# Optimization experiments

Measured on AMD Instinct MI355X. Metric: run time of the kernel, lower is better.

The kernel has to match this reference:

```python
import jax, jax.numpy as jnp
import numpy as np

# DeltaNet single-token decode step. Hard-coded dims from the torch source:
# hidden H=2048 (chosen), qk=2048 (16h x 128 -> repeat to 32h), v=4096 (32h x 128),
# conv channels 8192, kernel 4, state [1,32,128,128].
H = 2048
EPS = 1e-6

def _l2norm(x):
    return x * jax.lax.rsqrt(jnp.sum(x * x, axis=-1, keepdims=True) + EPS)

def setup_inputs() -> dict:
    key = jax.random.key(0)
    ks = jax.random.split(key, 12)
    w = lambda k, s, sc=0.02: jax.random.normal(k, s, dtype=jnp.float32) * sc
    return {
        "x": jax.random.normal(ks[0], (1, 1, H), dtype=jnp.float32),
        "state": jax.random.normal(ks[1], (1, 32, 128, 128), dtype=jnp.float32) * 0.02,
        "conv_state": jax.random.normal(ks[2], (1, 8192, 3), dtype=jnp.float32) * 0.1,
        "W_qkv": w(ks[3], (8192, H)),
        "W_z": w(ks[4], (4096, H)),
        "W_b": w(ks[5], (32, H)),
        "W_a": w(ks[6], (32, H)),
        "conv_w": w(ks[7], (8192, 1, 4), 0.3),
        "A_log": jax.random.uniform(ks[8], (32,), minval=-2.0, maxval=0.0, dtype=jnp.float32),
        "dt_bias": w(ks[9], (32,), 0.5),
        "norm_w": jnp.ones((128,), jnp.float32),
        "W_out": w(ks[10], (H, 4096)),
    }

def reference(x, state, conv_state, W_qkv, W_z, W_b, W_a, conv_w, A_log, dt_bias, norm_w, W_out):
    # projections (bias-free Linear, torch convention y = x @ W.T)
    mixed = jnp.einsum('blh,ch->blc', x, W_qkv)           # [1,1,8192]
    z = jnp.einsum('blh,ch->blc', x, W_z).reshape(1, 1, 32, 128)
    beta = jax.nn.sigmoid(jnp.einsum('blh,ch->blc', x, W_b))  # [1,1,32]
    a = jnp.einsum('blh,ch->blc', x, W_a)                 # [1,1,32]

    # depthwise causal conv (groups=8192, kernel 4, output length 1)
    combined = jnp.concatenate([conv_state, mixed.transpose(0, 2, 1)], axis=-1)  # [1,8192,4]
    new_conv = combined[:, :, -3:]
    conv_out = jnp.sum(combined * conv_w[None, :, 0, :], axis=-1)  # [1,8192]
    mixed = jax.nn.silu(conv_out)[:, None, :]             # [1,1,8192]

    q, k, v = mixed[..., :2048], mixed[..., 2048:4096], mixed[..., 4096:]
    q = jnp.repeat(q.reshape(1, 1, 16, 128), 2, axis=2)   # [1,1,32,128]
    k = jnp.repeat(k.reshape(1, 1, 16, 128), 2, axis=2)
    v = v.reshape(1, 1, 32, 128)

    g = -jnp.exp(A_log) * jax.nn.softplus(a + dt_bias)    # [1,1,32]

    q = _l2norm(q)[:, 0] / jnp.sqrt(jnp.float32(128.0))   # [1,32,128]
    k = _l2norm(k)[:, 0]
    v = v[:, 0]
    g_t = jnp.exp(g[:, 0])[..., None, None]               # [1,32,1,1]
    beta_t = beta[:, 0][..., None]                        # [1,32,1]

    # gated delta-rule state update
    s = state * g_t                                       # [1,32,128,128]
    kv_mem = jnp.einsum('bhkv,bhk->bhv', s, k)            # [1,32,128]
    delta = (v - kv_mem) * beta_t
    new_state = s + k[..., None] * delta[..., None, :]    # [1,32,128,128]
    out = jnp.einsum('bhkv,bhk->bhv', new_state, q)       # [1,32,128]

    # gated RMSNorm (Mamba2-style: rmsnorm(x * silu(z)) * w)
    out_flat = out.reshape(-1, 128)
    z_flat = z.reshape(-1, 128)
    gated = out_flat * jax.nn.silu(z_flat)
    out_flat = gated * jax.lax.rsqrt(jnp.mean(gated * gated, axis=-1, keepdims=True) + EPS) * norm_w

    out = jnp.einsum('blc,hc->blh', out_flat.reshape(1, 1, 4096), W_out)  # [1,1,H]
    return (out, new_state, new_conv)
```

## Files before the change

### kernel.cpp

```cpp
#include <hip/hip_runtime.h>
#include <math.h>

__device__ __forceinline__ float silu(float x){ return x / (1.f + expf(-x)); }

__global__ __launch_bounds__(256) void k_gemv_in(
    const float* __restrict__ x,
    const float* __restrict__ Wqkv,
    const float* __restrict__ Wz,
    const float* __restrict__ Wb,
    const float* __restrict__ Wa,
    float* __restrict__ mixed, float* __restrict__ zb,
    float* __restrict__ b_raw, float* __restrict__ a_raw)
{
  const int tid  = threadIdx.x;
  const int lane = tid & 63;
  const int wave = tid >> 6;

  float4 xr[8];
  #pragma unroll
  for (int j = 0; j < 8; j++)
    xr[j] = *(const float4*)(x + j*256 + lane*4);

  const int row0 = blockIdx.x * 8 + wave * 2;
  const float* W; float* dst;
  if (row0 < 8192)       { W = Wqkv + (size_t)row0 * 2048;          dst = mixed + row0; }
  else if (row0 < 12288) { W = Wz   + (size_t)(row0-8192) * 2048;   dst = zb + (row0-8192); }
  else if (row0 < 12320) { W = Wb   + (size_t)(row0-12288) * 2048;  dst = b_raw + (row0-12288); }
  else                   { W = Wa   + (size_t)(row0-12320) * 2048;  dst = a_raw + (row0-12320); }

  float acc0 = 0.f, acc1 = 0.f;
  #pragma unroll
  for (int j = 0; j < 8; j++){
    float4 w0 = *(const float4*)(W + j*256 + lane*4);
    float4 w1 = *(const float4*)(W + 2048 + j*256 + lane*4);
    acc0 += w0.x*xr[j].x + w0.y*xr[j].y + w0.z*xr[j].z + w0.w*xr[j].w;
    acc1 += w1.x*xr[j].x + w1.y*xr[j].y + w1.z*xr[j].z + w1.w*xr[j].w;
  }
  #pragma unroll
  for (int off = 32; off >= 1; off >>= 1){
    acc0 += __shfl_xor(acc0, off, 64);
    acc1 += __shfl_xor(acc1, off, 64);
  }
  if (lane == 0){ dst[0] = acc0; dst[1] = acc1; }
}

__global__ __launch_bounds__(256) void k_head(
    const float* __restrict__ mixed,
    const float* __restrict__ conv_state,
    const float* __restrict__ conv_w,
    const float* __restrict__ zbuf,
    const float* __restrict__ b_raw,
    const float* __restrict__ a_raw,
    const float* __restrict__ A_log,
    const float* __restrict__ dt_bias,
    const float* __restrict__ norm_w,
    const float* __restrict__ state,
    const float* __restrict__ Wout,
    float* __restrict__ new_state,
    float* __restrict__ new_conv,
    float* __restrict__ out_flat,
    float* __restrict__ scratch)
{
  const int b   = blockIdx.x;
  const int tid = threadIdx.x;

  if (b >= 32){
    const float4* W4 = (const float4*)Wout + (size_t)b * 8192;
    float4 a = make_float4(0.f, 0.f, 0.f, 0.f);
    #pragma unroll
    for (int j = 0; j < 32; j++){
      float4 w = W4[j*256 + tid];
      a.x += w.x; a.y += w.y; a.z += w.z; a.w += w.w;
    }
    if (tid == 0) scratch[b] = a.x + a.y + a.z + a.w;
    return;
  }

  const int h  = b;
  const int hb = h >> 1;
  const int t  = tid & 127;
  const int lane = tid & 63, wid = tid >> 6;

  __shared__ float qn[128], kn[128];
  __shared__ __align__(16) float vs[128];
  __shared__ float4 kvp[8][32];
  __shared__ float red[4];

  float qv = 0.f, kv = 0.f;
  if (tid < 128){
    int c = hb*128 + t;
    float c0 = conv_state[c*3+0], c1 = conv_state[c*3+1], c2 = conv_state[c*3+2];
    float m  = mixed[c];
    qv = silu(c0*conv_w[c*4+0] + c1*conv_w[c*4+1] + c2*conv_w[c*4+2] + m*conv_w[c*4+3]);
    new_conv[c*3+0] = c1; new_conv[c*3+1] = c2; new_conv[c*3+2] = m;
    c = 2048 + hb*128 + t;
    c0 = conv_state[c*3+0]; c1 = conv_state[c*3+1]; c2 = conv_state[c*3+2];
    m  = mixed[c];
    kv = silu(c0*conv_w[c*4+0] + c1*conv_w[c*4+1] + c2*conv_w[c*4+2] + m*conv_w[c*4+3]);
    new_conv[c*3+0] = c1; new_conv[c*3+1] = c2; new_conv[c*3+2] = m;

    float sq = qv*qv, sk = kv*kv;
    #pragma unroll
    for (int off = 32; off >= 1; off >>= 1){
      sq += __shfl_xor(sq, off, 64);
      sk += __shfl_xor(sk, off, 64);
    }
    if (lane == 0){ red[wid] = sq; red[2+wid] = sk; }
  } else {
    int c = 4096 + h*128 + t;
    float c0 = conv_state[c*3+0], c1 = conv_state[c*3+1], c2 = conv_state[c*3+2];
    float m  = mixed[c];
    vs[t] = silu(c0*conv_w[c*4+0] + c1*conv_w[c*4+1] + c2*conv_w[c*4+2] + m*conv_w[c*4+3]);
    new_conv[c*3+0] = c1; new_conv[c*3+1] = c2; new_conv[c*3+2] = m;
  }
  __syncthreads();
  const float qscale = rsqrtf(red[0]+red[1] + 1e-6f) * 0.088388347648318440550f;
  const float kscale = rsqrtf(red[2]+red[3] + 1e-6f);
  if (tid < 128){ qn[t] = qv * qscale; kn[t] = kv * kscale; }
  __syncthreads();

  float g_t, beta;
  {
    const float av = a_raw[h] + dt_bias[h];
    const float sp = (av > 20.f) ? av : log1pf(expf(av));
    g_t  = expf(-expf(A_log[h]) * sp);
    beta = 1.f / (1.f + expf(-b_raw[h]));
  }

  const int cg = tid & 31, part = tid >> 5;
  const int k0 = part * 16;
  const float* st  = state     + (size_t)h * 16384;
  float*       nst = new_state + (size_t)h * 16384;

  float4 s4[16];
  float4 kvm = make_float4(0.f, 0.f, 0.f, 0.f);
  #pragma unroll
  for (int i = 0; i < 16; i++){
    float4 sv = *(const float4*)(st + (k0+i)*128 + cg*4);
    sv.x *= g_t; sv.y *= g_t; sv.z *= g_t; sv.w *= g_t;
    s4[i] = sv;
    const float kk = kn[k0+i];
    kvm.x += sv.x*kk; kvm.y += sv.y*kk; kvm.z += sv.z*kk; kvm.w += sv.w*kk;
  }
  kvp[part][cg] = kvm;
  __syncthreads();
  float4 kt = make_float4(0.f, 0.f, 0.f, 0.f);
  #pragma unroll
  for (int p = 0; p < 8; p++){
    float4 kp = kvp[p][cg];
    kt.x += kp.x; kt.y += kp.y; kt.z += kp.z; kt.w += kp.w;
  }
  const float4 v4 = *(const float4*)(vs + cg*4);
  float4 delta;
  delta.x = (v4.x - kt.x) * beta;
  delta.y = (v4.y - kt.y) * beta;
  delta.z = (v4.z - kt.z) * beta;
  delta.w = (v4.w - kt.w) * beta;

  float4 oacc = make_float4(0.f, 0.f, 0.f, 0.f);
  #pragma unroll
  for (int i = 0; i < 16; i++){
    const float kk = kn[k0+i];
    float4 ns;
    ns.x = s4[i].x + kk*delta.x;
    ns.y = s4[i].y + kk*delta.y;
    ns.z = s4[i].z + kk*delta.z;
    ns.w = s4[i].w + kk*delta.w;
    *(float4*)(nst + (k0+i)*128 + cg*4) = ns;
    const float qq = qn[k0+i];
    oacc.x += ns.x*qq; oacc.y += ns.y*qq; oacc.z += ns.z*qq; oacc.w += ns.w*qq;
  }
  __syncthreads();
  kvp[part][cg] = oacc;
  __syncthreads();
  if (part == 0){
    float4 o = make_float4(0.f, 0.f, 0.f, 0.f);
    #pragma unroll
    for (int p = 0; p < 8; p++){
      float4 op = kvp[p][cg];
      o.x += op.x; o.y += op.y; o.z += op.z; o.w += op.w;
    }
    const float4 z4 = *(const float4*)(zbuf + h*128 + cg*4);
    float4 g4;
    g4.x = o.x * silu(z4.x);
    g4.y = o.y * silu(z4.y);
    g4.z = o.z * silu(z4.z);
    g4.w = o.w * silu(z4.w);
    float s2 = g4.x*g4.x + g4.y*g4.y + g4.z*g4.z + g4.w*g4.w;
    #pragma unroll
    for (int off = 16; off >= 1; off >>= 1) s2 += __shfl_xor(s2, off, 64);
    const float r = rsqrtf(s2 * (1.f/128.f) + 1e-6f);
    const float4 nw = *(const float4*)(norm_w + cg*4);
    float4 ov;
    ov.x = g4.x * r * nw.x;
    ov.y = g4.y * r * nw.y;
    ov.z = g4.z * r * nw.z;
    ov.w = g4.w * r * nw.w;
    *(float4*)(out_flat + h*128 + cg*4) = ov;
  }
}

__global__ __launch_bounds__(256) void k_gemv_out(
    const float* __restrict__ out_flat,
    const float* __restrict__ Wout,
    float* __restrict__ out)
{
  __shared__ float xs[4096];
  const int tid = threadIdx.x;
  #pragma unroll
  for (int i = 0; i < 4; i++)
    *(float4*)(xs + tid*4 + i*1024) = *(const float4*)(out_flat + tid*4 + i*1024);
  __syncthreads();

  const int lane = tid & 63, wave = tid >> 6;
  const int row0 = blockIdx.x * 8 + wave * 2;
  const float* W0 = Wout + (size_t)row0 * 4096;
  float acc0 = 0.f, acc1 = 0.f;
  #pragma unroll
  for (int j = 0; j < 16; j++){
    float4 w0 = *(const float4*)(W0 + j*256 + lane*4);
    float4 w1 = *(const float4*)(W0 + 4096 + j*256 + lane*4);
    const float x0 = xs[j*256+lane*4+0], x1 = xs[j*256+lane*4+1];
    const float x2 = xs[j*256+lane*4+2], x3 = xs[j*256+lane*4+3];
    acc0 += w0.x*x0 + w0.y*x1 + w0.z*x2 + w0.w*x3;
    acc1 += w1.x*x0 + w1.y*x1 + w1.z*x2 + w1.w*x3;
  }
  #pragma unroll
  for (int off = 32; off >= 1; off >>= 1){
    acc0 += __shfl_xor(acc0, off, 64);
    acc1 += __shfl_xor(acc1, off, 64);
  }
  if (lane == 0){ out[row0] = acc0; out[row0+1] = acc1; }
}

extern "C" void kernel_launch(void* const* d_in, const int* in_sizes, int n_in,
                              void* d_out, int out_size, void* d_ws, size_t ws_size,
                              hipStream_t stream) {
  const float* x          = (const float*)d_in[0];
  const float* state      = (const float*)d_in[1];
  const float* conv_state = (const float*)d_in[2];
  const float* W_qkv      = (const float*)d_in[3];
  const float* W_z        = (const float*)d_in[4];
  const float* W_b        = (const float*)d_in[5];
  const float* W_a        = (const float*)d_in[6];
  const float* conv_w     = (const float*)d_in[7];
  const float* A_log      = (const float*)d_in[8];
  const float* dt_bias    = (const float*)d_in[9];
  const float* norm_w     = (const float*)d_in[10];
  const float* W_out      = (const float*)d_in[11];

  float* out       = (float*)d_out;
  float* new_state = (float*)d_out + 2048;
  float* new_conv  = (float*)d_out + 2048 + 524288;

  float* ws      = (float*)d_ws;
  float* mixed   = ws;
  float* zb      = ws + 8192;
  float* b_raw   = ws + 12288;
  float* a_raw   = ws + 12320;
  float* oflat   = ws + 12352;
  float* scratch = ws + 16448;

  hipLaunchKernelGGL(k_gemv_in, dim3(1544), dim3(256), 0, stream,
                     x, W_qkv, W_z, W_b, W_a, mixed, zb, b_raw, a_raw);
  hipLaunchKernelGGL(k_head, dim3(256), dim3(256), 0, stream,
                     mixed, conv_state, conv_w, zb, b_raw, a_raw, A_log, dt_bias,
                     norm_w, state, W_out, new_state, new_conv, oflat, scratch);
  hipLaunchKernelGGL(k_gemv_out, dim3(256), dim3(256), 0, stream,
                     oflat, W_out, out);
}
```

Baseline: 177.8 us.

## Fuse three decode kernels into one cooperative persistent kernel with grid syncs

Merges the input GEMV, the per-head delta-rule update and the output GEMV into a single cooperative kernel of 256 blocks, with grid-wide syncs between stages. The input GEMV becomes a grid-stride loop over rows, and the W_out prefetch-warming pass now runs in every block before the final stage. The goal is to remove the inter-kernel launch gaps and keep W_out warm in cache. The trade-off is that the first GEMV now runs on far fewer blocks (256 instead of 1544), which can limit memory parallelism, and the grid syncs add their own overhead.

```diff
diff --git a/kernel.cpp b/kernel.cpp
--- a/kernel.cpp
+++ b/kernel.cpp
@@ -1,236 +1,236 @@
 #include <hip/hip_runtime.h>
+#include <hip/hip_cooperative_groups.h>
 #include <math.h>
 
+namespace cg = cooperative_groups;
+
 __device__ __forceinline__ float silu(float x){ return x / (1.f + expf(-x)); }
 
-__global__ __launch_bounds__(256) void k_gemv_in(
+__global__ __launch_bounds__(256) void k_fused(
     const float* __restrict__ x,
-    const float* __restrict__ Wqkv,
-    const float* __restrict__ Wz,
-    const float* __restrict__ Wb,
-    const float* __restrict__ Wa,
-    float* __restrict__ mixed, float* __restrict__ zb,
-    float* __restrict__ b_raw, float* __restrict__ a_raw)
-{
-  const int tid  = threadIdx.x;
-  const int lane = tid & 63;
-  const int wave = tid >> 6;
-
-  float4 xr[8];
-  #pragma unroll
-  for (int j = 0; j < 8; j++)
-    xr[j] = *(const float4*)(x + j*256 + lane*4);
-
-  const int row0 = blockIdx.x * 8 + wave * 2;
-  const float* W; float* dst;
-  if (row0 < 8192)       { W = Wqkv + (size_t)row0 * 2048;          dst = mixed + row0; }
-  else if (row0 < 12288) { W = Wz   + (size_t)(row0-8192) * 2048;   dst = zb + (row0-8192); }
-  else if (row0 < 12320) { W = Wb   + (size_t)(row0-12288) * 2048;  dst = b_raw + (row0-12288); }
-  else                   { W = Wa   + (size_t)(row0-12320) * 2048;  dst = a_raw + (row0-12320); }
-
-  float acc0 = 0.f, acc1 = 0.f;
-  #pragma unroll
-  for (int j = 0; j < 8; j++){
-    float4 w0 = *(const float4*)(W + j*256 + lane*4);
-    float4 w1 = *(const float4*)(W + 2048 + j*256 + lane*4);
-    acc0 += w0.x*xr[j].x + w0.y*xr[j].y + w0.z*xr[j].z + w0.w*xr[j].w;
-    acc1 += w1.x*xr[j].x + w1.y*xr[j].y + w1.z*xr[j].z + w1.w*xr[j].w;
-  }
-  #pragma unroll
-  for (int off = 32; off >= 1; off >>= 1){
-    acc0 += __shfl_xor(acc0, off, 64);
-    acc1 += __shfl_xor(acc1, off, 64);
-  }
-  if (lane == 0){ dst[0] = acc0; dst[1] = acc1; }
-}
-
-__global__ __launch_bounds__(256) void k_head(
-    const float* __restrict__ mixed,
     const float* __restrict__ conv_state,
+    const float* __restrict__ W_qkv,
+    const float* __restrict__ W_z,
+    const float* __restrict__ W_b,
+    const float* __restrict__ W_a,
     const float* __restrict__ conv_w,
-    const float* __restrict__ zbuf,
-    const float* __restrict__ b_raw,
-    const float* __restrict__ a_raw,
     const float* __restrict__ A_log,
     const float* __restrict__ dt_bias,
     const float* __restrict__ norm_w,
     const float* __restrict__ state,
     const float* __restrict__ Wout,
+    float* __restrict__ out,
     float* __restrict__ new_state,
     float* __restrict__ new_conv,
-    float* __restrict__ out_flat,
+    float* __restrict__ mixed,
+    float* __restrict__ zb,
+    float* __restrict__ b_raw,
+    float* __restrict__ a_raw,
+    float* __restrict__ oflat,
     float* __restrict__ scratch)
 {
-  const int b   = blockIdx.x;
-  const int tid = threadIdx.x;
-
-  if (b >= 32){
-    const float4* W4 = (const float4*)Wout + (size_t)b * 8192;
-    float4 a = make_float4(0.f, 0.f, 0.f, 0.f);
-    #pragma unroll
-    for (int j = 0; j < 32; j++){
-      float4 w = W4[j*256 + tid];
-      a.x += w.x; a.y += w.y; a.z += w.z; a.w += w.w;
-    }
-    if (tid == 0) scratch[b] = a.x + a.y + a.z + a.w;
-    return;
-  }
-
-  const int h  = b;
-  const int hb = h >> 1;
-  const int t  = tid & 127;
-  const int lane = tid & 63, wid = tid >> 6;
+  cg::grid_group grid = cg::this_grid();
+  const int b    = blockIdx.x;
+  const int tid  = threadIdx.x;
+  const int lane = tid & 63;
+  const int wave = tid >> 6;
 
   __shared__ float qn[128], kn[128];
   __shared__ __align__(16) float vs[128];
   __shared__ float4 kvp[8][32];
   __shared__ float red[4];
-
-  float qv = 0.f, kv = 0.f;
-  if (tid < 128){
-    int c = hb*128 + t;
-    float c0 = conv_state[c*3+0], c1 = conv_state[c*3+1], c2 = conv_state[c*3+2];
-    float m  = mixed[c];
-    qv = silu(c0*conv_w[c*4+0] + c1*conv_w[c*4+1] + c2*conv_w[c*4+2] + m*conv_w[c*4+3]);
-    new_conv[c*3+0] = c1; new_conv[c*3+1] = c2; new_conv[c*3+2] = m;
-    c = 2048 + hb*128 + t;
-    c0 = conv_state[c*3+0]; c1 = conv_state[c*3+1]; c2 = conv_state[c*3+2];
-    m  = mixed[c];
-    kv = silu(c0*conv_w[c*4+0] + c1*conv_w[c*4+1] + c2*conv_w[c*4+2] + m*conv_w[c*4+3]);
-    new_conv[c*3+0] = c1; new_conv[c*3+1] = c2; new_conv[c*3+2] = m;
-
-    float sq = qv*qv, sk = kv*kv;
+  __shared__ __align__(16) float xs[4096];
+
+  {
+    float4 xr[8];
+    #pragma unroll
+    for (int j = 0; j < 8; j++)
+      xr[j] = *(const float4*)(x + j*256 + lane*4);
+
+    for (int row0 = (b*4 + wave)*2; row0 < 12352; row0 += 2048){
+      const float* W; float* dst;
+      if (row0 < 8192)       { W = W_qkv + (size_t)row0 * 2048;          dst = mixed + row0; }
+      else if (row0 < 12288) { W = W_z   + (size_t)(row0-8192) * 2048;   dst = zb + (row0-8192); }
+      else if (row0 < 12320) { W = W_b   + (size_t)(row0-12288) * 2048;  dst = b_raw + (row0-12288); }
+      else                   { W = W_a   + (size_t)(row0-12320) * 2048;  dst = a_raw + (row0-12320); }
+
+      float acc0 = 0.f, acc1 = 0.f;
+      #pragma unroll
+      for (int j = 0; j < 8; j++){
+        float4 w0 = *(const float4*)(W + j*256 + lane*4);
+        float4 w1 = *(const float4*)(W + 2048 + j*256 + lane*4);
+        acc0 += w0.x*xr[j].x + w0.y*xr[j].y + w0.z*xr[j].z + w0.w*xr[j].w;
+        acc1 += w1.x*xr[j].x + w1.y*xr[j].y + w1.z*xr[j].z + w1.w*xr[j].w;
+      }
+      #pragma unroll
+      for (int off = 32; off >= 1; off >>= 1){
+        acc0 += __shfl_xor(acc0, off, 64);
+        acc1 += __shfl_xor(acc1, off, 64);
+      }
+      if (lane == 0){ dst[0] = acc0; dst[1] = acc1; }
+    }
+  }
+
+  grid.sync();
+
+  if (b < 32){
+    const int h  = b;
+    const int hb = h >> 1;
+    const int t  = tid & 127;
+    const int wid = tid >> 6;
+
+    float qv = 0.f, kv = 0.f;
+    if (tid < 128){
+      int c = hb*128 + t;
+      float c0 = conv_state[c*3+0], c1 = conv_state[c*3+1], c2 = conv_state[c*3+2];
+      float m  = mixed[c];
+      qv = silu(c0*conv_w[c*4+0] + c1*conv_w[c*4+1] + c2*conv_w[c*4+2] + m*conv_w[c*4+3]);
+      new_conv[c*3+0] = c1; new_conv[c*3+1] = c2; new_conv[c*3+2] = m;
+      c = 2048 + hb*128 + t;
+      c0 = conv_state[c*3+0]; c1 = conv_state[c*3+1]; c2 = conv_state[c*3+2];
+      m  = mixed[c];
+      kv = silu(c0*conv_w[c*4+0] + c1*conv_w[c*4+1] + c2*conv_w[c*4+2] + m*conv_w[c*4+3]);
+      new_conv[c*3+0] = c1; new_conv[c*3+1] = c2; new_conv[c*3+2] = m;
+
+      float sq = qv*qv, sk = kv*kv;
+      #pragma unroll
+      for (int off = 32; off >= 1; off >>= 1){
+        sq += __shfl_xor(sq, off, 64);
+        sk += __shfl_xor(sk, off, 64);
+      }
+      if (lane == 0){ red[wid] = sq; red[2+wid] = sk; }
+    } else {
+      int c = 4096 + h*128 + t;
+      float c0 = conv_state[c*3+0], c1 = conv_state[c*3+1], c2 = conv_state[c*3+2];
+      float m  = mixed[c];
+      vs[t] = silu(c0*conv_w[c*4+0] + c1*conv_w[c*4+1] + c2*conv_w[c*4+2] + m*conv_w[c*4+3]);
+      new_conv[c*3+0] = c1; new_conv[c*3+1] = c2; new_conv[c*3+2] = m;
+    }
+    __syncthreads();
+    const float qscale = rsqrtf(red[0]+red[1] + 1e-6f) * 0.088388347648318440550f;
+    const float kscale = rsqrtf(red[2]+red[3] + 1e-6f);
+    if (tid < 128){ qn[t] = qv * qscale; kn[t] = kv * kscale; }
+    __syncthreads();
+
+    float g_t, beta;
+    {
+      const float av = a_raw[h] + dt_bias[h];
+      const float sp = (av > 20.f) ? av : log1pf(expf(av));
+      g_t  = expf(-expf(A_log[h]) * sp);
+      beta = 1.f / (1.f + expf(-b_raw[h]));
+    }
+
+    const int cg_ = tid & 31, part = tid >> 5;
+    const int k0 = part * 16;
+    const float* st  = state     + (size_t)h * 16384;
+    float*       nst = new_state + (size_t)h * 16384;
+
+    float4 s4[16];
+    float4 kvm = make_float4(0.f, 0.f, 0.f, 0.f);
+    #pragma unroll
+    for (int i = 0; i < 16; i++){
+      float4 sv = *(const float4*)(st + (k0+i)*128 + cg_*4);
+      sv.x *= g_t; sv.y *= g_t; sv.z *= g_t; sv.w *= g_t;
+      s4[i] = sv;
+      const float kk = kn[k0+i];
+      kvm.x += sv.x*kk; kvm.y += sv.y*kk; kvm.z += sv.z*kk; kvm.w += sv.w*kk;
+    }
+    kvp[part][cg_] = kvm;
+    __syncthreads();
+    float4 kt = make_float4(0.f, 0.f, 0.f, 0.f);
+    #pragma unroll
+    for (int p = 0; p < 8; p++){
+      float4 kp = kvp[p][cg_];
+      kt.x += kp.x; kt.y += kp.y; kt.z += kp.z; kt.w += kp.w;
+    }
+    const float4 v4 = *(const float4*)(vs + cg_*4);
+    float4 delta;
+    delta.x = (v4.x - kt.x) * beta;
+    delta.y = (v4.y - kt.y) * beta;
+    delta.z = (v4.z - kt.z) * beta;
+    delta.w = (v4.w - kt.w) * beta;
+
+    float4 oacc = make_float4(0.f, 0.f, 0.f, 0.f);
+    #pragma unroll
+    for (int i = 0; i < 16; i++){
+      const float kk = kn[k0+i];
+      float4 ns;
+      ns.x = s4[i].x + kk*delta.x;
+      ns.y = s4[i].y + kk*delta.y;
+      ns.z = s4[i].z + kk*delta.z;
+      ns.w = s4[i].w + kk*delta.w;
+      *(float4*)(nst + (k0+i)*128 + cg_*4) = ns;
+      const float qq = qn[k0+i];
+      oacc.x += ns.x*qq; oacc.y += ns.y*qq; oacc.z += ns.z*qq; oacc.w += ns.w*qq;
+    }
+    __syncthreads();
+    kvp[part][cg_] = oacc;
+    __syncthreads();
+    if (part == 0){
+      float4 o = make_float4(0.f, 0.f, 0.f, 0.f);
+      #pragma unroll
+      for (int p = 0; p < 8; p++){
+        float4 op = kvp[p][cg_];
+        o.x += op.x; o.y += op.y; o.z += op.z; o.w += op.w;
+      }
+      const float4 z4 = *(const float4*)(zb + h*128 + cg_*4);
+      float4 g4;
+      g4.x = o.x * silu(z4.x);
+      g4.y = o.y * silu(z4.y);
+      g4.z = o.z * silu(z4.z);
+      g4.w = o.w * silu(z4.w);
+      float s2 = g4.x*g4.x + g4.y*g4.y + g4.z*g4.z + g4.w*g4.w;
+      #pragma unroll
+      for (int off = 16; off >= 1; off >>= 1) s2 += __shfl_xor(s2, off, 64);
+      const float r = rsqrtf(s2 * (1.f/128.f) + 1e-6f);
+      const float4 nw = *(const float4*)(norm_w + cg_*4);
+      float4 ov;
+      ov.x = g4.x * r * nw.x;
+      ov.y = g4.y * r * nw.y;
+      ov.z = g4.z * r * nw.z;
+      ov.w = g4.w * r * nw.w;
+      *(float4*)(oflat + h*128 + cg_*4) = ov;
+    }
+  }
+
+  {
+    const float4* W4 = (const float4*)Wout + (size_t)b * 8192;
+    float4 a = make_float4(0.f, 0.f, 0.f, 0.f);
+    #pragma unroll
+    for (int j = 0; j < 32; j++){
+      float4 w = W4[j*256 + tid];
+      a.x += w.x; a.y += w.y; a.z += w.z; a.w += w.w;
+    }
+    if (tid == 0) scratch[b] = a.x + a.y + a.z + a.w;
+  }
+
+  grid.sync();
+
+  {
+    #pragma unroll
+    for (int i = 0; i < 4; i++)
+      *(float4*)(xs + tid*4 + i*1024) = *(const float4*)(oflat + tid*4 + i*1024);
+    __syncthreads();
+
+    const int row0 = b * 8 + wave * 2;
+    const float* W0 = Wout + (size_t)row0 * 4096;
+    float acc0 = 0.f, acc1 = 0.f;
+    #pragma unroll
+    for (int j = 0; j < 16; j++){
+      float4 w0 = *(const float4*)(W0 + j*256 + lane*4);
+      float4 w1 = *(const float4*)(W0 + 4096 + j*256 + lane*4);
+      const float x0 = xs[j*256+lane*4+0], x1 = xs[j*256+lane*4+1];
+      const float x2 = xs[j*256+lane*4+2], x3 = xs[j*256+lane*4+3];
+      acc0 += w0.x*x0 + w0.y*x1 + w0.z*x2 + w0.w*x3;
+      acc1 += w1.x*x0 + w1.y*x1 + w1.z*x2 + w1.w*x3;
+    }
     #pragma unroll
     for (int off = 32; off >= 1; off >>= 1){
-      sq += __shfl_xor(sq, off, 64);
-      sk += __shfl_xor(sk, off, 64);
-    }
-    if (lane == 0){ red[wid] = sq; red[2+wid] = sk; }
-  } else {
-    int c = 4096 + h*128 + t;
-    float c0 = conv_state[c*3+0], c1 = conv_state[c*3+1], c2 = conv_state[c*3+2];
-    float m  = mixed[c];
-    vs[t] = silu(c0*conv_w[c*4+0] + c1*conv_w[c*4+1] + c2*conv_w[c*4+2] + m*conv_w[c*4+3]);
-    new_conv[c*3+0] = c1; new_conv[c*3+1] = c2; new_conv[c*3+2] = m;
-  }
-  __syncthreads();
-  const float qscale = rsqrtf(red[0]+red[1] + 1e-6f) * 0.088388347648318440550f;
-  const float kscale = rsqrtf(red[2]+red[3] + 1e-6f);
-  if (tid < 128){ qn[t] = qv * qscale; kn[t] = kv * kscale; }
-  __syncthreads();
-
-  float g_t, beta;
-  {
-    const float av = a_raw[h] + dt_bias[h];
-    const float sp = (av > 20.f) ? av : log1pf(expf(av));
-    g_t  = expf(-expf(A_log[h]) * sp);
-    beta = 1.f / (1.f + expf(-b_raw[h]));
-  }
-
-  const int cg = tid & 31, part = tid >> 5;
-  const int k0 = part * 16;
-  const float* st  = state     + (size_t)h * 16384;
-  float*       nst = new_state + (size_t)h * 16384;
-
-  float4 s4[16];
-  float4 kvm = make_float4(0.f, 0.f, 0.f, 0.f);
-  #pragma unroll
-  for (int i = 0; i < 16; i++){
-    float4 sv = *(const float4*)(st + (k0+i)*128 + cg*4);
-    sv.x *= g_t; sv.y *= g_t; sv.z *= g_t; sv.w *= g_t;
-    s4[i] = sv;
-    const float kk = kn[k0+i];
-    kvm.x += sv.x*kk; kvm.y += sv.y*kk; kvm.z += sv.z*kk; kvm.w += sv.w*kk;
-  }
-  kvp[part][cg] = kvm;
-  __syncthreads();
-  float4 kt = make_float4(0.f, 0.f, 0.f, 0.f);
-  #pragma unroll
-  for (int p = 0; p < 8; p++){
-    float4 kp = kvp[p][cg];
-    kt.x += kp.x; kt.y += kp.y; kt.z += kp.z; kt.w += kp.w;
-  }
-  const float4 v4 = *(const float4*)(vs + cg*4);
-  float4 delta;
-  delta.x = (v4.x - kt.x) * beta;
-  delta.y = (v4.y - kt.y) * beta;
-  delta.z = (v4.z - kt.z) * beta;
-  delta.w = (v4.w - kt.w) * beta;
-
-  float4 oacc = make_float4(0.f, 0.f, 0.f, 0.f);
-  #pragma unroll
-  for (int i = 0; i < 16; i++){
-    const float kk = kn[k0+i];
-    float4 ns;
-    ns.x = s4[i].x + kk*delta.x;
-    ns.y = s4[i].y + kk*delta.y;
-    ns.z = s4[i].z + kk*delta.z;
-    ns.w = s4[i].w + kk*delta.w;
-    *(float4*)(nst + (k0+i)*128 + cg*4) = ns;
-    const float qq = qn[k0+i];
-    oacc.x += ns.x*qq; oacc.y += ns.y*qq; oacc.z += ns.z*qq; oacc.w += ns.w*qq;
-  }
-  __syncthreads();
-  kvp[part][cg] = oacc;
-  __syncthreads();
-  if (part == 0){
-    float4 o = make_float4(0.f, 0.f, 0.f, 0.f);
-    #pragma unroll
-    for (int p = 0; p < 8; p++){
-      float4 op = kvp[p][cg];
-      o.x += op.x; o.y += op.y; o.z += op.z; o.w += op.w;
-    }
-    const float4 z4 = *(const float4*)(zbuf + h*128 + cg*4);
-    float4 g4;
-    g4.x = o.x * silu(z4.x);
-    g4.y = o.y * silu(z4.y);
-    g4.z = o.z * silu(z4.z);
-    g4.w = o.w * silu(z4.w);
-    float s2 = g4.x*g4.x + g4.y*g4.y + g4.z*g4.z + g4.w*g4.w;
-    #pragma unroll
-    for (int off = 16; off >= 1; off >>= 1) s2 += __shfl_xor(s2, off, 64);
-    const float r = rsqrtf(s2 * (1.f/128.f) + 1e-6f);
-    const float4 nw = *(const float4*)(norm_w + cg*4);
-    float4 ov;
-    ov.x = g4.x * r * nw.x;
-    ov.y = g4.y * r * nw.y;
-    ov.z = g4.z * r * nw.z;
-    ov.w = g4.w * r * nw.w;
-    *(float4*)(out_flat + h*128 + cg*4) = ov;
-  }
-}
-
-__global__ __launch_bounds__(256) void k_gemv_out(
-    const float* __restrict__ out_flat,
-    const float* __restrict__ Wout,
-    float* __restrict__ out)
-{
-  __shared__ float xs[4096];
-  const int tid = threadIdx.x;
-  #pragma unroll
-  for (int i = 0; i < 4; i++)
-    *(float4*)(xs + tid*4 + i*1024) = *(const float4*)(out_flat + tid*4 + i*1024);
-  __syncthreads();
-
-  const int lane = tid & 63, wave = tid >> 6;
-  const int row0 = blockIdx.x * 8 + wave * 2;
-  const float* W0 = Wout + (size_t)row0 * 4096;
-  float acc0 = 0.f, acc1 = 0.f;
-  #pragma unroll
-  for (int j = 0; j < 16; j++){
-    float4 w0 = *(const float4*)(W0 + j*256 + lane*4);
-    float4 w1 = *(const float4*)(W0 + 4096 + j*256 + lane*4);
-    const float x0 = xs[j*256+lane*4+0], x1 = xs[j*256+lane*4+1];
-    const float x2 = xs[j*256+lane*4+2], x3 = xs[j*256+lane*4+3];
-    acc0 += w0.x*x0 + w0.y*x1 + w0.z*x2 + w0.w*x3;
-    acc1 += w1.x*x0 + w1.y*x1 + w1.z*x2 + w1.w*x3;
-  }
-  #pragma unroll
-  for (int off = 32; off >= 1; off >>= 1){
-    acc0 += __shfl_xor(acc0, off, 64);
-    acc1 += __shfl_xor(acc1, off, 64);
-  }
-  if (lane == 0){ out[row0] = acc0; out[row0+1] = acc1; }
+      acc0 += __shfl_xor(acc0, off, 64);
+      acc1 += __shfl_xor(acc1, off, 64);
+    }
+    if (lane == 0){ out[row0] = acc0; out[row0+1] = acc1; }
+  }
 }
 
 extern "C" void kernel_launch(void* const* d_in, const int* in_sizes, int n_in,
@@ -261,11 +261,14 @@
   float* oflat   = ws + 12352;
   float* scratch = ws + 16448;
 
-  hipLaunchKernelGGL(k_gemv_in, dim3(1544), dim3(256), 0, stream,
-                     x, W_qkv, W_z, W_b, W_a, mixed, zb, b_raw, a_raw);
-  hipLaunchKernelGGL(k_head, dim3(256), dim3(256), 0, stream,
-                     mixed, conv_state, conv_w, zb, b_raw, a_raw, A_log, dt_bias,
-                     norm_w, state, W_out, new_state, new_conv, oflat, scratch);
-  hipLaunchKernelGGL(k_gemv_out, dim3(256), dim3(256), 0, stream,
-                     oflat, W_out, out);
+  void* args[] = {
+    (void*)&x, (void*)&conv_state, (void*)&W_qkv, (void*)&W_z, (void*)&W_b,
+    (void*)&W_a, (void*)&conv_w, (void*)&A_log, (void*)&dt_bias, (void*)&norm_w,
+    (void*)&state, (void*)&W_out,
+    (void*)&out, (void*)&new_state, (void*)&new_conv,
+    (void*)&mixed, (void*)&zb, (void*)&b_raw, (void*)&a_raw, (void*)&oflat,
+    (void*)&scratch
+  };
+  hipLaunchCooperativeKernel((const void*)k_fused, dim3(256), dim3(256),
+                             args, 0, stream);
 }
```

Measured after the change: 266.9 us. 50.1% more time.
